# Kernel optimization log

Hardware: AMD Instinct MI355X
Metric: run time of the kernel (lower is better)

The kernel has to match this reference:

```python
import jax, jax.numpy as jnp
import numpy as np

NUM_HEADS = 16
THETA = 10000.0

def _apply_rope(x, positions):
    # x: [B, H, S, dh] with interleaved pairs; positions: [B, S] int
    dh = x.shape[-1]
    inv_freq = THETA ** (-jnp.arange(0, dh, 2, dtype=jnp.float32) / dh)  # [dh/2]
    ang = positions.astype(jnp.float32)[:, None, :, None] * inv_freq  # [B,1,S,dh/2]
    cos, sin = jnp.cos(ang), jnp.sin(ang)
    x1, x2 = x[..., 0::2], x[..., 1::2]
    out_even = x1 * cos - x2 * sin
    out_odd = x1 * sin + x2 * cos
    return jnp.stack([out_even, out_odd], axis=-1).reshape(x.shape)

def setup_inputs() -> dict:
    B, S, D = 2, 2048, 2048
    key = jax.random.key(0)
    ks = jax.random.split(key, 5)
    scale = 0.02
    inp = {
        'in_features': jax.random.normal(ks[0], (B, S, D), dtype=jnp.float32),
        'token_positions': jnp.broadcast_to(jnp.arange(S, dtype=jnp.int32), (B, S)),
        'mask': jnp.tril(jnp.ones((S, S), dtype=bool)),
        'q_proj_weight': jax.random.normal(ks[1], (D, D), dtype=jnp.float32) * scale,
        'k_proj_weight': jax.random.normal(ks[2], (D, D), dtype=jnp.float32) * scale,
        'v_proj_weight': jax.random.normal(ks[3], (D, D), dtype=jnp.float32) * scale,
        'o_proj_weight': jax.random.normal(ks[4], (D, D), dtype=jnp.float32) * scale,
    }
    return inp

def reference(in_features, token_positions, mask, q_proj_weight, k_proj_weight, v_proj_weight, o_proj_weight):
    B, S, d_in = in_features.shape
    d_k = q_proj_weight.shape[0]
    d_v = v_proj_weight.shape[0]
    H = NUM_HEADS
    dk_head, dv_head = d_k // H, d_v // H
    Q = jnp.einsum('bsd,kd->bsk', in_features, q_proj_weight).reshape(B, S, H, dk_head).transpose(0, 2, 1, 3)
    K = jnp.einsum('bsd,kd->bsk', in_features, k_proj_weight).reshape(B, S, H, dk_head).transpose(0, 2, 1, 3)
    V = jnp.einsum('bsd,vd->bsv', in_features, v_proj_weight).reshape(B, S, H, dv_head).transpose(0, 2, 1, 3)
    Q = _apply_rope(Q, token_positions)
    K = _apply_rope(K, token_positions)
    scores = jnp.einsum('bhqd,bhkd->bhqk', Q, K) / jnp.sqrt(jnp.float32(dk_head))
    scores = jnp.where(mask[None, None, :, :], scores, jnp.finfo(scores.dtype).min)
    attn = jax.nn.softmax(scores, axis=-1)
    out = jnp.einsum('bhqk,bhkd->bhqd', attn, V)  # [B,H,S,dv_head]
    out = out.transpose(0, 2, 1, 3).reshape(B, S, d_v)
    return jnp.einsum('bsv,mv->bsm', out, o_proj_weight)
```

## Files before the change

kernel.cpp:

```cpp
#include <hip/hip_runtime.h>
#include <hip/hip_bf16.h>
#include <cstdint>

typedef __bf16 bf16_t;
typedef __bf16 bf16x8 __attribute__((ext_vector_type(8)));
typedef __bf16 bf16x4 __attribute__((ext_vector_type(4)));
typedef float  f32x4  __attribute__((ext_vector_type(4)));

#define B_  2
#define S_  2048
#define D_  2048
#define H_  16
#define DH_ 128
#define LDQ 6144

__device__ __forceinline__ void gload_lds16(const bf16_t* g, bf16_t* l) {
    __builtin_amdgcn_global_load_lds(
        (const __attribute__((address_space(1))) void*)g,
        (__attribute__((address_space(3))) void*)l, 16, 0, 0);
}

#define BAR  do { asm volatile("" ::: "memory"); __builtin_amdgcn_s_barrier(); \
                  asm volatile("" ::: "memory"); } while (0)
#define WAITLGKM do { asm volatile("s_waitcnt lgkmcnt(0)" ::: "memory"); \
                      __builtin_amdgcn_sched_barrier(0); } while (0)

__global__ __launch_bounds__(256)
void cast_all_k(const float* __restrict__ X,  const float* __restrict__ Wq,
                const float* __restrict__ Wk, const float* __restrict__ Wv,
                const float* __restrict__ Wo,
                bf16_t* __restrict__ Xb, bf16_t* __restrict__ Wqkv,
                bf16_t* __restrict__ Wob) {
    long bid = blockIdx.x;
    const float* src; bf16_t* dst; long off;
    if      (bid <  8192) { src = X;  dst = Xb;             off = bid;         }
    else if (bid < 12288) { src = Wq; dst = Wqkv;           off = bid - 8192;  }
    else if (bid < 16384) { src = Wk; dst = Wqkv + 4194304; off = bid - 12288; }
    else if (bid < 20480) { src = Wv; dst = Wqkv + 8388608; off = bid - 16384; }
    else                  { src = Wo; dst = Wob;            off = bid - 20480; }
    long i = (off * 256 + threadIdx.x) * 4;
    float4 v = *(const float4*)(src + i);
    bf16x4 o = {(bf16_t)v.x, (bf16_t)v.y, (bf16_t)v.z, (bf16_t)v.w};
    *(bf16x4*)(dst + i) = o;
}

#define LDS8(s, row, chunk) \
    (*(const bf16x8*)((s) + (row) * 64 + ((((chunk) ^ ((row) & 7))) << 3)))

#define MMQ(mh, nh, bfx) \
    _Pragma("unroll") for (int mi = 0; mi < 4; ++mi) { \
      _Pragma("unroll") for (int ni = 0; ni < 2; ++ni) { \
        _Pragma("unroll") for (int ks = 0; ks < 2; ++ks) \
          acc[(mh)*4+mi][(nh)*2+ni] = __builtin_amdgcn_mfma_f32_16x16x32_bf16( \
              af[mi][ks], bfx[ni][ks], acc[(mh)*4+mi][(nh)*2+ni], 0, 0, 0); } }

__device__ __forceinline__ void ktile8(
    const bf16_t* sAc, const bf16_t* sBc,
    bf16_t* sAn, bf16_t* sBn,
    bool do_stage, long k0s,
    const bf16_t* Agp, const bf16_t* Bgp, int lda, int ldb,
    int wm, int wn, int fr, int hi, int w,
    f32x4 acc[8][4]) {
    bf16x8 af[4][2], bf0[2][2], bf1[2][2];
#pragma unroll
    for (int mi = 0; mi < 4; ++mi)
#pragma unroll
        for (int ks = 0; ks < 2; ++ks)
            af[mi][ks] = LDS8(sAc, wm * 128 + mi * 16 + fr, ks * 4 + hi);
#pragma unroll
    for (int ni = 0; ni < 2; ++ni)
#pragma unroll
        for (int ks = 0; ks < 2; ++ks)
            bf0[ni][ks] = LDS8(sBc, wn * 64 + ni * 16 + fr, ks * 4 + hi);
    if (do_stage) {
#pragma unroll
        for (int p = 0; p < 4; ++p)
            gload_lds16(Agp + (long)(p * 64) * lda + k0s, sAn + p * 4096 + w * 512);
    }
    BAR; WAITLGKM;
    __builtin_amdgcn_s_setprio(1);
    MMQ(0, 0, bf0);
    __builtin_amdgcn_s_setprio(0);
    BAR;
#pragma unroll
    for (int ni = 0; ni < 2; ++ni)
#pragma unroll
        for (int ks = 0; ks < 2; ++ks)
            bf1[ni][ks] = LDS8(sBc, wn * 64 + 32 + ni * 16 + fr, ks * 4 + hi);
    if (do_stage) {
#pragma unroll
        for (int p = 0; p < 4; ++p)
            gload_lds16(Bgp + (long)(p * 64) * ldb + k0s, sBn + p * 4096 + w * 512);
    }
    BAR; WAITLGKM;
    __builtin_amdgcn_s_setprio(1);
    MMQ(0, 1, bf1);
    __builtin_amdgcn_s_setprio(0);
    BAR;
#pragma unroll
    for (int mi = 0; mi < 4; ++mi)
#pragma unroll
        for (int ks = 0; ks < 2; ++ks)
            af[mi][ks] = LDS8(sAc, wm * 128 + 64 + mi * 16 + fr, ks * 4 + hi);
    BAR; WAITLGKM;
    __builtin_amdgcn_s_setprio(1);
    MMQ(1, 0, bf0);
    __builtin_amdgcn_s_setprio(0);
    BAR;
    __builtin_amdgcn_s_setprio(1);
    MMQ(1, 1, bf1);
    __builtin_amdgcn_s_setprio(0);
    if (do_stage) asm volatile("s_waitcnt vmcnt(0)" ::: "memory");
    BAR;
}

template<bool C_BF16>
__global__ __launch_bounds__(512, 1)
void gemm_nt8(const bf16_t* __restrict__ A, int lda,
              const bf16_t* __restrict__ B, int ldb,
              void* __restrict__ Cp, int ldc, int K, int nbx) {
    __shared__ bf16_t sA[2][256 * 64];
    __shared__ bf16_t sB[2][256 * 64];
    const int tid  = threadIdx.x;
    const int w    = tid >> 6;
    const int lane = tid & 63;
    const int fr   = lane & 15;
    const int hi   = lane >> 4;
    const int wm   = w >> 2;
    const int wn   = w & 3;

    const int nwg = gridDim.x;
    const int lin = blockIdx.x;
    const int swz = (lin & 7) * (nwg >> 3) + (lin >> 3);
    const long bm = (long)(swz / nbx) * 256;
    const long bn = (long)(swz % nbx) * 256;

    const int  srow = tid >> 3;
    const int  scol = ((tid & 7) ^ (srow & 7)) * 8;
    const bf16_t* Agp = A + (bm + srow) * (long)lda + scol;
    const bf16_t* Bgp = B + (bn + srow) * (long)ldb + scol;

    f32x4 acc[8][4] = {};
    const int nkt = K >> 6;

#pragma unroll
    for (int p = 0; p < 4; ++p)
        gload_lds16(Agp + (long)(p * 64) * lda, sA[0] + p * 4096 + w * 512);
#pragma unroll
    for (int p = 0; p < 4; ++p)
        gload_lds16(Bgp + (long)(p * 64) * ldb, sB[0] + p * 4096 + w * 512);
    asm volatile("s_waitcnt vmcnt(0)" ::: "memory");
    BAR;

    for (int kt = 0; kt < nkt; kt += 2) {
        ktile8(sA[0], sB[0], sA[1], sB[1], true, (long)(kt + 1) << 6,
               Agp, Bgp, lda, ldb, wm, wn, fr, hi, w, acc);
        ktile8(sA[1], sB[1], sA[0], sB[0], (kt + 2) < nkt, (long)(kt + 2) << 6,
               Agp, Bgp, lda, ldb, wm, wn, fr, hi, w, acc);
    }

#pragma unroll
    for (int m = 0; m < 8; ++m) {
        long r0 = bm + wm * 128 + m * 16 + hi * 4;
#pragma unroll
        for (int n = 0; n < 4; ++n) {
            long cc = bn + wn * 64 + n * 16 + fr;
#pragma unroll
            for (int v = 0; v < 4; ++v) {
                if (C_BF16)
                    ((bf16_t*)Cp)[(r0 + v) * (long)ldc + cc] = (bf16_t)acc[m][n][v];
                else
                    ((float*)Cp)[(r0 + v) * (long)ldc + cc] = acc[m][n][v];
            }
        }
    }
}

__global__ __launch_bounds__(256)
void rope_qk_k(bf16_t* __restrict__ QKV, const int* __restrict__ pos) {
    int t = blockIdx.x * 256 + threadIdx.x;
    int g = t & 15;
    int h = (t >> 4) & 15;
    int s = (t >> 8) & 2047;
    int b = t >> 19;
    long qa = ((long)(b * S_ + s)) * LDQ + h * DH_ + g * 8;
    long ka = qa + D_;
    float p = (float)pos[b * S_ + s];
    bf16x8 q = *(bf16x8*)(QKV + qa);
    bf16x8 k = *(bf16x8*)(QKV + ka);
#pragma unroll
    for (int e = 0; e < 4; ++e) {
        int i = g * 4 + e;
        float invf = exp2f(-(float)i * 0.20762050593045702f);
        float ang = p * invf;
        float sn, cs;
        __sincosf(ang, &sn, &cs);
        float q1 = (float)q[2 * e], q2 = (float)q[2 * e + 1];
        q[2 * e]     = (bf16_t)(q1 * cs - q2 * sn);
        q[2 * e + 1] = (bf16_t)(q1 * sn + q2 * cs);
        float k1 = (float)k[2 * e], k2 = (float)k[2 * e + 1];
        k[2 * e]     = (bf16_t)(k1 * cs - k2 * sn);
        k[2 * e + 1] = (bf16_t)(k1 * sn + k2 * cs);
    }
    *(bf16x8*)(QKV + qa) = q;
    *(bf16x8*)(QKV + ka) = k;
}

__global__ __launch_bounds__(256)
void transpose_v_k(const bf16_t* __restrict__ QKV, bf16_t* __restrict__ Vt) {
    __shared__ bf16_t tile[64][80];
    int t = threadIdx.x;
    int bh = blockIdx.z;
    int b = bh >> 4, h = bh & 15;
    long s0 = (long)blockIdx.x * 64;
    int d0 = blockIdx.y * 64;
    const bf16_t* src = QKV + ((long)b * S_ + s0) * LDQ + 2 * D_ + h * DH_ + d0;
#pragma unroll
    for (int p = 0; p < 2; ++p) {
        int r = (t >> 3) + p * 32;
        int c = (t & 7) * 8;
        *(bf16x8*)&tile[r][c] = *(const bf16x8*)&src[(long)r * LDQ + c];
    }
    __syncthreads();
    bf16_t* dst = Vt + ((long)bh * DH_ + d0) * S_ + s0;
#pragma unroll
    for (int p = 0; p < 2; ++p) {
        int d = (t >> 3) + p * 32;
        int c = (t & 7) * 8;
        bf16x8 v;
#pragma unroll
        for (int e = 0; e < 8; ++e) v[e] = tile[c + e][d];
        *(bf16x8*)&dst[(long)d * S_ + c] = v;
    }
}

__device__ __forceinline__ bf16x8 ldsw(const bf16_t* p, int row, int ecol) {
    return *(const bf16x8*)(p + row * 128 + (ecol ^ ((row & 7) << 3)));
}

__global__ __launch_bounds__(512, 1)
void flash_attn_k(const bf16_t* __restrict__ QKV, const bf16_t* __restrict__ Vt,
                  bf16_t* __restrict__ O) {
    __shared__ bf16_t Ksh[2][128 * 128];
    __shared__ bf16_t Vsh[2][128 * 128];
    __shared__ bf16_t Psh[128 * 128];

    const int tid  = threadIdx.x;
    const int w    = tid >> 6;
    const int lane = tid & 63;
    const int fr   = lane & 15;
    const int hi   = lane >> 4;
    const int hi8  = hi * 8;
    const int hi4  = hi * 4;
    const int w16  = w * 16;

    const int bid = blockIdx.x;
    const int qi  = 15 - (bid >> 5);
    const int bh  = bid & 31;
    const int b   = bh >> 4;
    const int h   = bh & 15;
    const long bS   = (long)b * S_;
    const int  qoff = h * DH_;
    const int  koff = D_ + h * DH_;
    const long vbase = (long)bh * DH_;

#pragma unroll
    for (int p = 0; p < 4; ++p) {
        int idx = p * 512 + tid;
        int row = idx >> 4;
        int sl  = (idx & 15) ^ (row & 7);
        gload_lds16(QKV + (bS + qi * 128 + row) * (long)LDQ + qoff + sl * 8,
                    &Psh[(p * 512 + w * 64) * 8]);
    }
#pragma unroll
    for (int p = 0; p < 4; ++p) {
        int idx = p * 512 + tid;
        int row = idx >> 4;
        int sl  = (idx & 15) ^ (row & 7);
        gload_lds16(QKV + (bS + row) * (long)LDQ + koff + sl * 8,
                    &Ksh[0][(p * 512 + w * 64) * 8]);
        gload_lds16(Vt + (vbase + row) * S_ + sl * 8,
                    &Vsh[0][(p * 512 + w * 64) * 8]);
    }
    asm volatile("s_waitcnt vmcnt(8)" ::: "memory");
    __builtin_amdgcn_s_barrier();
    asm volatile("" ::: "memory");

    bf16x8 qfrag[4];
#pragma unroll
    for (int kk = 0; kk < 4; ++kk)
        qfrag[kk] = ldsw(Psh, w16 + fr, kk * 32 + hi8);

    f32x4 o[8] = {};
    float m_run[4] = {-3.0e38f, -3.0e38f, -3.0e38f, -3.0e38f};
    float l_run[4] = {};

    const float SC = 0.08838834764831845f * 1.4426950408889634f;

    for (int kt = 0; kt <= qi; ++kt) {
        const int buf = kt & 1;
        if (kt < qi) {
#pragma unroll
            for (int p = 0; p < 4; ++p) {
                int idx = p * 512 + tid;
                int row = idx >> 4;
                int sl  = (idx & 15) ^ (row & 7);
                gload_lds16(QKV + (bS + (kt + 1) * 128 + row) * (long)LDQ + koff + sl * 8,
                            &Ksh[buf ^ 1][(p * 512 + w * 64) * 8]);
                gload_lds16(Vt + (vbase + row) * S_ + (kt + 1) * 128 + sl * 8,
                            &Vsh[buf ^ 1][(p * 512 + w * 64) * 8]);
            }
            asm volatile("s_waitcnt vmcnt(8)" ::: "memory");
        } else {
            asm volatile("s_waitcnt vmcnt(0)" ::: "memory");
        }
        __builtin_amdgcn_s_barrier();
        asm volatile("" ::: "memory");

        f32x4 sc[8];
#pragma unroll
        for (int j = 0; j < 8; ++j) {
            f32x4 z = {};
#pragma unroll
            for (int kk = 0; kk < 4; ++kk)
                z = __builtin_amdgcn_mfma_f32_16x16x32_bf16(
                        qfrag[kk], ldsw(Ksh[buf], j * 16 + fr, kk * 32 + hi8), z, 0, 0, 0);
            sc[j] = z;
        }

        const bool diag = (kt == qi);
#pragma unroll
        for (int j = 0; j < 8; ++j)
#pragma unroll
            for (int v = 0; v < 4; ++v) {
                float x = sc[j][v] * SC;
                if (diag && (j * 16 + fr > w16 + hi4 + v)) x = -3.0e38f;
                sc[j][v] = x;
            }

        float fsc[4];
#pragma unroll
        for (int v = 0; v < 4; ++v) {
            float m = fmaxf(fmaxf(fmaxf(sc[0][v], sc[1][v]), fmaxf(sc[2][v], sc[3][v])),
                            fmaxf(fmaxf(sc[4][v], sc[5][v]), fmaxf(sc[6][v], sc[7][v])));
            m = fmaxf(m, __shfl_xor(m, 1));
            m = fmaxf(m, __shfl_xor(m, 2));
            m = fmaxf(m, __shfl_xor(m, 4));
            m = fmaxf(m, __shfl_xor(m, 8));
            float mn = fmaxf(m_run[v], m);
            fsc[v] = exp2f(m_run[v] - mn);
            m_run[v] = mn;
            l_run[v] *= fsc[v];
        }
#pragma unroll
        for (int j2 = 0; j2 < 8; ++j2)
#pragma unroll
            for (int v = 0; v < 4; ++v) o[j2][v] *= fsc[v];

#pragma unroll
        for (int j = 0; j < 8; ++j)
#pragma unroll
            for (int v = 0; v < 4; ++v) {
                float p = exp2f(sc[j][v] - m_run[v]);
                l_run[v] += p;
                int row = w16 + hi4 + v;
                int col = j * 16 + fr;
                Psh[row * 128 + (col ^ ((row & 7) << 3))] = (bf16_t)p;
            }

        asm volatile("s_waitcnt lgkmcnt(0)" ::: "memory");
        __builtin_amdgcn_sched_barrier(0);

        bf16x8 pa[4];
#pragma unroll
        for (int kk = 0; kk < 4; ++kk)
            pa[kk] = ldsw(Psh, w16 + fr, kk * 32 + hi8);
#pragma unroll
        for (int j2 = 0; j2 < 8; ++j2)
#pragma unroll
            for (int kk = 0; kk < 4; ++kk)
                o[j2] = __builtin_amdgcn_mfma_f32_16x16x32_bf16(
                            pa[kk], ldsw(Vsh[buf], j2 * 16 + fr, kk * 32 + hi8), o[j2], 0, 0, 0);

        asm volatile("" ::: "memory");
        __builtin_amdgcn_s_barrier();
        asm volatile("" ::: "memory");
    }

#pragma unroll
    for (int v = 0; v < 4; ++v) {
        float l = l_run[v];
        l += __shfl_xor(l, 1);
        l += __shfl_xor(l, 2);
        l += __shfl_xor(l, 4);
        l += __shfl_xor(l, 8);
        l_run[v] = 1.0f / l;
    }
    const long orow = bS + qi * 128 + w16 + hi4;
#pragma unroll
    for (int j2 = 0; j2 < 8; ++j2)
#pragma unroll
        for (int v = 0; v < 4; ++v)
            O[(orow + v) * D_ + qoff + j2 * 16 + fr] = (bf16_t)(o[j2][v] * l_run[v]);
}

extern "C" void kernel_launch(void* const* d_in, const int* in_sizes, int n_in,
                              void* d_out, int out_size, void* d_ws, size_t ws_size,
                              hipStream_t stream) {
    const float* in_features = (const float*)d_in[0];
    const int*   positions   = (const int*)d_in[1];
    const float* Wq = (const float*)d_in[3];
    const float* Wk = (const float*)d_in[4];
    const float* Wv = (const float*)d_in[5];
    const float* Wo = (const float*)d_in[6];
    float* out = (float*)d_out;

    const size_t SZ_X   = (size_t)B_ * S_ * D_ * 2;
    const size_t SZ_W   = (size_t)D_ * D_ * 2;
    const size_t SZ_QKV = (size_t)B_ * S_ * LDQ * 2;
    if (ws_size < SZ_X * 3 + SZ_W * 4 + SZ_QKV) return;

    char* w = (char*)d_ws;
    bf16_t* Xb      = (bf16_t*)w;   w += SZ_X;
    bf16_t* Wqkv    = (bf16_t*)w;   w += SZ_W * 3;
    bf16_t* Wob     = (bf16_t*)w;   w += SZ_W;
    bf16_t* QKV     = (bf16_t*)w;   w += SZ_QKV;
    bf16_t* Vt      = (bf16_t*)w;   w += SZ_X;
    bf16_t* AttnOut = (bf16_t*)w;   w += SZ_X;

    cast_all_k<<<24576, 256, 0, stream>>>(in_features, Wq, Wk, Wv, Wo, Xb, Wqkv, Wob);

    gemm_nt8<true><<<384, 512, 0, stream>>>(Xb, D_, Wqkv, D_, QKV, LDQ, D_, 24);

    rope_qk_k<<<4096, 256, 0, stream>>>(QKV, positions);
    transpose_v_k<<<dim3(32, 2, 32), 256, 0, stream>>>(QKV, Vt);

    flash_attn_k<<<512, 512, 0, stream>>>(QKV, Vt, AttnOut);

    gemm_nt8<false><<<128, 512, 0, stream>>>(AttnOut, D_, Wob, D_, out, D_, D_, 8);
}
```

Before: 425.9 us.

## Split GEMM tile staging into finer quarter-tile prefetches and retile output projection

Replaces the two-tile ktile8 GEMM with a templated kernel that issues global-to-LDS loads in half-tile pieces spread across the four MFMA phases. A wait on all but the two most recent loads replaces the full vmcnt(0) wait, so loads can stay in flight across iterations. The output projection GEMM changes to a 256x128 tile with 4x2 warps and 256 blocks, giving more workgroups to fill the CUs. The finer-grained buffer reuse depends on the barrier and waitcnt ordering, which adds a risk of races on the LDS buffers.

```diff
diff --git a/kernel.cpp b/kernel.cpp
--- a/kernel.cpp
+++ b/kernel.cpp
@@ -47,123 +47,148 @@
 #define LDS8(s, row, chunk) \
     (*(const bf16x8*)((s) + (row) * 64 + ((((chunk) ^ ((row) & 7))) << 3)))
 
-#define MMQ(mh, nh, bfx) \
-    _Pragma("unroll") for (int mi = 0; mi < 4; ++mi) { \
-      _Pragma("unroll") for (int ni = 0; ni < 2; ++ni) { \
-        _Pragma("unroll") for (int ks = 0; ks < 2; ++ks) \
-          acc[(mh)*4+mi][(nh)*2+ni] = __builtin_amdgcn_mfma_f32_16x16x32_bf16( \
-              af[mi][ks], bfx[ni][ks], acc[(mh)*4+mi][(nh)*2+ni], 0, 0, 0); } }
-
-__device__ __forceinline__ void ktile8(
-    const bf16_t* sAc, const bf16_t* sBc,
-    bf16_t* sAn, bf16_t* sBn,
-    bool do_stage, long k0s,
-    const bf16_t* Agp, const bf16_t* Bgp, int lda, int ldb,
-    int wm, int wn, int fr, int hi, int w,
-    f32x4 acc[8][4]) {
-    bf16x8 af[4][2], bf0[2][2], bf1[2][2];
-#pragma unroll
-    for (int mi = 0; mi < 4; ++mi)
-#pragma unroll
-        for (int ks = 0; ks < 2; ++ks)
-            af[mi][ks] = LDS8(sAc, wm * 128 + mi * 16 + fr, ks * 4 + hi);
-#pragma unroll
-    for (int ni = 0; ni < 2; ++ni)
-#pragma unroll
-        for (int ks = 0; ks < 2; ++ks)
-            bf0[ni][ks] = LDS8(sBc, wn * 64 + ni * 16 + fr, ks * 4 + hi);
-    if (do_stage) {
-#pragma unroll
-        for (int p = 0; p < 4; ++p)
-            gload_lds16(Agp + (long)(p * 64) * lda + k0s, sAn + p * 4096 + w * 512);
-    }
-    BAR; WAITLGKM;
-    __builtin_amdgcn_s_setprio(1);
-    MMQ(0, 0, bf0);
-    __builtin_amdgcn_s_setprio(0);
-    BAR;
-#pragma unroll
-    for (int ni = 0; ni < 2; ++ni)
-#pragma unroll
-        for (int ks = 0; ks < 2; ++ks)
-            bf1[ni][ks] = LDS8(sBc, wn * 64 + 32 + ni * 16 + fr, ks * 4 + hi);
-    if (do_stage) {
-#pragma unroll
-        for (int p = 0; p < 4; ++p)
-            gload_lds16(Bgp + (long)(p * 64) * ldb + k0s, sBn + p * 4096 + w * 512);
-    }
-    BAR; WAITLGKM;
-    __builtin_amdgcn_s_setprio(1);
-    MMQ(0, 1, bf1);
-    __builtin_amdgcn_s_setprio(0);
-    BAR;
-#pragma unroll
-    for (int mi = 0; mi < 4; ++mi)
-#pragma unroll
-        for (int ks = 0; ks < 2; ++ks)
-            af[mi][ks] = LDS8(sAc, wm * 128 + 64 + mi * 16 + fr, ks * 4 + hi);
-    BAR; WAITLGKM;
-    __builtin_amdgcn_s_setprio(1);
-    MMQ(1, 0, bf0);
-    __builtin_amdgcn_s_setprio(0);
-    BAR;
-    __builtin_amdgcn_s_setprio(1);
-    MMQ(1, 1, bf1);
-    __builtin_amdgcn_s_setprio(0);
-    if (do_stage) asm volatile("s_waitcnt vmcnt(0)" ::: "memory");
-    BAR;
-}
-
-template<bool C_BF16>
+template<bool C_BF16, int BM, int BN, int WMG, int WNG>
 __global__ __launch_bounds__(512, 1)
-void gemm_nt8(const bf16_t* __restrict__ A, int lda,
+void gemm_nt9(const bf16_t* __restrict__ A, int lda,
               const bf16_t* __restrict__ B, int ldb,
               void* __restrict__ Cp, int ldc, int K, int nbx) {
-    __shared__ bf16_t sA[2][256 * 64];
-    __shared__ bf16_t sB[2][256 * 64];
+    constexpr int WTM = BM / WMG;
+    constexpr int MR  = WTM / 16;
+    constexpr int NR  = 4;
+    constexpr int MH  = MR / 2;
+    constexpr int NH  = 2;
+    constexpr int LA  = BM / 128;
+    constexpr int LB  = BN / 128;
+    __shared__ bf16_t sA[2][BM * 64];
+    __shared__ bf16_t sB[2][BN * 64];
+
     const int tid  = threadIdx.x;
     const int w    = tid >> 6;
     const int lane = tid & 63;
     const int fr   = lane & 15;
     const int hi   = lane >> 4;
-    const int wm   = w >> 2;
-    const int wn   = w & 3;
+    const int wm   = w / WNG;
+    const int wn   = w % WNG;
 
     const int nwg = gridDim.x;
     const int lin = blockIdx.x;
     const int swz = (lin & 7) * (nwg >> 3) + (lin >> 3);
-    const long bm = (long)(swz / nbx) * 256;
-    const long bn = (long)(swz % nbx) * 256;
-
-    const int  srow = tid >> 3;
-    const int  scol = ((tid & 7) ^ (srow & 7)) * 8;
+    const long bm = (long)(swz / nbx) * BM;
+    const long bn = (long)(swz % nbx) * BN;
+
+    const int srow = tid >> 3;
+    const int scol = ((tid & 7) ^ (srow & 7)) * 8;
     const bf16_t* Agp = A + (bm + srow) * (long)lda + scol;
     const bf16_t* Bgp = B + (bn + srow) * (long)ldb + scol;
 
-    f32x4 acc[8][4] = {};
+#define STAGE_A(bsel, h, kt) { _Pragma("unroll") \
+    for (int p = 0; p < LA; ++p) \
+        gload_lds16(Agp + (long)((h) * (BM / 2) + p * 64) * lda + ((long)(kt) << 6), \
+                    &sA[bsel][((h) * (BM / 2) + p * 64) * 64 + w * 512]); }
+#define STAGE_B(bsel, h, kt) { _Pragma("unroll") \
+    for (int p = 0; p < LB; ++p) \
+        gload_lds16(Bgp + (long)((h) * (BN / 2) + p * 64) * ldb + ((long)(kt) << 6), \
+                    &sB[bsel][((h) * (BN / 2) + p * 64) * 64 + w * 512]); }
+
+    f32x4 acc[MR][NR] = {};
     const int nkt = K >> 6;
 
-#pragma unroll
-    for (int p = 0; p < 4; ++p)
-        gload_lds16(Agp + (long)(p * 64) * lda, sA[0] + p * 4096 + w * 512);
-#pragma unroll
-    for (int p = 0; p < 4; ++p)
-        gload_lds16(Bgp + (long)(p * 64) * ldb, sB[0] + p * 4096 + w * 512);
-    asm volatile("s_waitcnt vmcnt(0)" ::: "memory");
+    STAGE_A(0, 0, 0) STAGE_A(0, 1, 0)
+    STAGE_B(0, 0, 0) STAGE_B(0, 1, 0)
+    if (nkt > 1) STAGE_A(1, 0, 1)
+    asm volatile("s_waitcnt vmcnt(2)" ::: "memory");
     BAR;
 
-    for (int kt = 0; kt < nkt; kt += 2) {
-        ktile8(sA[0], sB[0], sA[1], sB[1], true, (long)(kt + 1) << 6,
-               Agp, Bgp, lda, ldb, wm, wn, fr, hi, w, acc);
-        ktile8(sA[1], sB[1], sA[0], sB[0], (kt + 2) < nkt, (long)(kt + 2) << 6,
-               Agp, Bgp, lda, ldb, wm, wn, fr, hi, w, acc);
-    }
-
-#pragma unroll
-    for (int m = 0; m < 8; ++m) {
-        long r0 = bm + wm * 128 + m * 16 + hi * 4;
-#pragma unroll
-        for (int n = 0; n < 4; ++n) {
+    for (int t = 0; t < nkt; ++t) {
+        const int c = t & 1;
+        const bf16_t* sAc = sA[c];
+        const bf16_t* sBc = sB[c];
+        const bool st1 = t + 1 < nkt;
+        const bool st2 = t + 2 < nkt;
+        bf16x8 af[MH][2], ag[MH][2], bf0[NH][2], bf1[NH][2];
+
+#pragma unroll
+        for (int mi = 0; mi < MH; ++mi)
+#pragma unroll
+            for (int ks = 0; ks < 2; ++ks)
+                af[mi][ks] = LDS8(sAc, wm * WTM + mi * 16 + fr, ks * 4 + hi);
+#pragma unroll
+        for (int ni = 0; ni < NH; ++ni)
+#pragma unroll
+            for (int ks = 0; ks < 2; ++ks)
+                bf0[ni][ks] = LDS8(sBc, wn * 64 + ni * 16 + fr, ks * 4 + hi);
+        if (st1) STAGE_A(c ^ 1, 1, t + 1)
+        BAR; WAITLGKM;
+        __builtin_amdgcn_s_setprio(1);
+#pragma unroll
+        for (int mi = 0; mi < MH; ++mi)
+#pragma unroll
+            for (int ni = 0; ni < NH; ++ni)
+#pragma unroll
+                for (int ks = 0; ks < 2; ++ks)
+                    acc[mi][ni] = __builtin_amdgcn_mfma_f32_16x16x32_bf16(
+                        af[mi][ks], bf0[ni][ks], acc[mi][ni], 0, 0, 0);
+        __builtin_amdgcn_s_setprio(0);
+        BAR;
+
+#pragma unroll
+        for (int ni = 0; ni < NH; ++ni)
+#pragma unroll
+            for (int ks = 0; ks < 2; ++ks)
+                bf1[ni][ks] = LDS8(sBc, wn * 64 + 32 + ni * 16 + fr, ks * 4 + hi);
+        if (st1) STAGE_B(c ^ 1, 0, t + 1)
+        BAR; WAITLGKM;
+        __builtin_amdgcn_s_setprio(1);
+#pragma unroll
+        for (int mi = 0; mi < MH; ++mi)
+#pragma unroll
+            for (int ni = 0; ni < NH; ++ni)
+#pragma unroll
+                for (int ks = 0; ks < 2; ++ks)
+                    acc[mi][NH + ni] = __builtin_amdgcn_mfma_f32_16x16x32_bf16(
+                        af[mi][ks], bf1[ni][ks], acc[mi][NH + ni], 0, 0, 0);
+        __builtin_amdgcn_s_setprio(0);
+        BAR;
+
+#pragma unroll
+        for (int mi = 0; mi < MH; ++mi)
+#pragma unroll
+            for (int ks = 0; ks < 2; ++ks)
+                ag[mi][ks] = LDS8(sAc, wm * WTM + (MH + mi) * 16 + fr, ks * 4 + hi);
+        if (st1) STAGE_B(c ^ 1, 1, t + 1)
+        BAR; WAITLGKM;
+        __builtin_amdgcn_s_setprio(1);
+#pragma unroll
+        for (int mi = 0; mi < MH; ++mi)
+#pragma unroll
+            for (int ni = 0; ni < NH; ++ni)
+#pragma unroll
+                for (int ks = 0; ks < 2; ++ks)
+                    acc[MH + mi][ni] = __builtin_amdgcn_mfma_f32_16x16x32_bf16(
+                        ag[mi][ks], bf0[ni][ks], acc[MH + mi][ni], 0, 0, 0);
+        __builtin_amdgcn_s_setprio(0);
+        BAR;
+
+        if (st2) STAGE_A(c, 0, t + 2)
+        __builtin_amdgcn_s_setprio(1);
+#pragma unroll
+        for (int mi = 0; mi < MH; ++mi)
+#pragma unroll
+            for (int ni = 0; ni < NH; ++ni)
+#pragma unroll
+                for (int ks = 0; ks < 2; ++ks)
+                    acc[MH + mi][NH + ni] = __builtin_amdgcn_mfma_f32_16x16x32_bf16(
+                        ag[mi][ks], bf1[ni][ks], acc[MH + mi][NH + ni], 0, 0, 0);
+        __builtin_amdgcn_s_setprio(0);
+        asm volatile("s_waitcnt vmcnt(2)" ::: "memory");
+        BAR;
+    }
+
+#pragma unroll
+    for (int m = 0; m < MR; ++m) {
+        long r0 = bm + wm * WTM + m * 16 + hi * 4;
+#pragma unroll
+        for (int n = 0; n < NR; ++n) {
             long cc = bn + wn * 64 + n * 16 + fr;
 #pragma unroll
             for (int v = 0; v < 4; ++v) {
@@ -174,6 +199,8 @@
             }
         }
     }
+#undef STAGE_A
+#undef STAGE_B
 }
 
 __global__ __launch_bounds__(256)
@@ -430,12 +457,14 @@
 
     cast_all_k<<<24576, 256, 0, stream>>>(in_features, Wq, Wk, Wv, Wo, Xb, Wqkv, Wob);
 
-    gemm_nt8<true><<<384, 512, 0, stream>>>(Xb, D_, Wqkv, D_, QKV, LDQ, D_, 24);
+    gemm_nt9<true, 256, 256, 2, 4><<<384, 512, 0, stream>>>(Xb, D_, Wqkv, D_,
+                                                            QKV, LDQ, D_, 24);
 
     rope_qk_k<<<4096, 256, 0, stream>>>(QKV, positions);
     transpose_v_k<<<dim3(32, 2, 32), 256, 0, stream>>>(QKV, Vt);
 
     flash_attn_k<<<512, 512, 0, stream>>>(QKV, Vt, AttnOut);
 
-    gemm_nt8<false><<<128, 512, 0, stream>>>(AttnOut, D_, Wob, D_, out, D_, D_, 8);
-}
+    gemm_nt9<false, 256, 128, 4, 2><<<256, 512, 0, stream>>>(AttnOut, D_, Wob, D_,
+                                                             out, D_, D_, 16);
+}
```

Measured after the change: 407.7 us. 4.3% less time.

## Restructure GEMM into per-k-tile loop with deeper staged prefetch and half-tile LDS

Applied to the files above, without the earlier changes.

Rewrites the bf16 GEMM main loop so each k-tile is processed in four MFMA quadrants, with global-to-LDS staging for tile t+2 issued into the buffer just consumed rather than t+1. LDS is split into half-tiles per warp row/column group, and the wait on outstanding loads becomes vmcnt(8) so one tile of prefetch stays in flight. The explicit lgkmcnt waits are removed, leaving barriers only. This aims to hide global load latency better and overlap it with MFMA work, at the risk of overwriting LDS still being read if the barrier ordering is insufficient.

```diff
diff --git a/kernel.cpp b/kernel.cpp
--- a/kernel.cpp
+++ b/kernel.cpp
@@ -22,8 +22,6 @@
 
 #define BAR  do { asm volatile("" ::: "memory"); __builtin_amdgcn_s_barrier(); \
                   asm volatile("" ::: "memory"); } while (0)
-#define WAITLGKM do { asm volatile("s_waitcnt lgkmcnt(0)" ::: "memory"); \
-                      __builtin_amdgcn_sched_barrier(0); } while (0)
 
 __global__ __launch_bounds__(256)
 void cast_all_k(const float* __restrict__ X,  const float* __restrict__ Wq,
@@ -47,80 +45,14 @@
 #define LDS8(s, row, chunk) \
     (*(const bf16x8*)((s) + (row) * 64 + ((((chunk) ^ ((row) & 7))) << 3)))
 
-#define MMQ(mh, nh, bfx) \
-    _Pragma("unroll") for (int mi = 0; mi < 4; ++mi) { \
-      _Pragma("unroll") for (int ni = 0; ni < 2; ++ni) { \
-        _Pragma("unroll") for (int ks = 0; ks < 2; ++ks) \
-          acc[(mh)*4+mi][(nh)*2+ni] = __builtin_amdgcn_mfma_f32_16x16x32_bf16( \
-              af[mi][ks], bfx[ni][ks], acc[(mh)*4+mi][(nh)*2+ni], 0, 0, 0); } }
-
-__device__ __forceinline__ void ktile8(
-    const bf16_t* sAc, const bf16_t* sBc,
-    bf16_t* sAn, bf16_t* sBn,
-    bool do_stage, long k0s,
-    const bf16_t* Agp, const bf16_t* Bgp, int lda, int ldb,
-    int wm, int wn, int fr, int hi, int w,
-    f32x4 acc[8][4]) {
-    bf16x8 af[4][2], bf0[2][2], bf1[2][2];
-#pragma unroll
-    for (int mi = 0; mi < 4; ++mi)
-#pragma unroll
-        for (int ks = 0; ks < 2; ++ks)
-            af[mi][ks] = LDS8(sAc, wm * 128 + mi * 16 + fr, ks * 4 + hi);
-#pragma unroll
-    for (int ni = 0; ni < 2; ++ni)
-#pragma unroll
-        for (int ks = 0; ks < 2; ++ks)
-            bf0[ni][ks] = LDS8(sBc, wn * 64 + ni * 16 + fr, ks * 4 + hi);
-    if (do_stage) {
-#pragma unroll
-        for (int p = 0; p < 4; ++p)
-            gload_lds16(Agp + (long)(p * 64) * lda + k0s, sAn + p * 4096 + w * 512);
-    }
-    BAR; WAITLGKM;
-    __builtin_amdgcn_s_setprio(1);
-    MMQ(0, 0, bf0);
-    __builtin_amdgcn_s_setprio(0);
-    BAR;
-#pragma unroll
-    for (int ni = 0; ni < 2; ++ni)
-#pragma unroll
-        for (int ks = 0; ks < 2; ++ks)
-            bf1[ni][ks] = LDS8(sBc, wn * 64 + 32 + ni * 16 + fr, ks * 4 + hi);
-    if (do_stage) {
-#pragma unroll
-        for (int p = 0; p < 4; ++p)
-            gload_lds16(Bgp + (long)(p * 64) * ldb + k0s, sBn + p * 4096 + w * 512);
-    }
-    BAR; WAITLGKM;
-    __builtin_amdgcn_s_setprio(1);
-    MMQ(0, 1, bf1);
-    __builtin_amdgcn_s_setprio(0);
-    BAR;
-#pragma unroll
-    for (int mi = 0; mi < 4; ++mi)
-#pragma unroll
-        for (int ks = 0; ks < 2; ++ks)
-            af[mi][ks] = LDS8(sAc, wm * 128 + 64 + mi * 16 + fr, ks * 4 + hi);
-    BAR; WAITLGKM;
-    __builtin_amdgcn_s_setprio(1);
-    MMQ(1, 0, bf0);
-    __builtin_amdgcn_s_setprio(0);
-    BAR;
-    __builtin_amdgcn_s_setprio(1);
-    MMQ(1, 1, bf1);
-    __builtin_amdgcn_s_setprio(0);
-    if (do_stage) asm volatile("s_waitcnt vmcnt(0)" ::: "memory");
-    BAR;
-}
-
 template<bool C_BF16>
 __global__ __launch_bounds__(512, 1)
-void gemm_nt8(const bf16_t* __restrict__ A, int lda,
-              const bf16_t* __restrict__ B, int ldb,
-              void* __restrict__ Cp, int ldc, int K, int nbx) {
-    __shared__ bf16_t sA[2][256 * 64];
-    __shared__ bf16_t sB[2][256 * 64];
+void gemm8(const bf16_t* __restrict__ A, int lda,
+           const bf16_t* __restrict__ B, int ldb,
+           void* __restrict__ Cp, int ldc, int K, int nbx) {
+    __shared__ bf16_t sA[2][2][128 * 64];
+    __shared__ bf16_t sB[2][2][128 * 64];
+
     const int tid  = threadIdx.x;
     const int w    = tid >> 6;
     const int lane = tid & 63;
@@ -128,6 +60,8 @@
     const int hi   = lane >> 4;
     const int wm   = w >> 2;
     const int wn   = w & 3;
+    const int bh2  = wn >> 1;
+    const int brow = (wn & 1) * 64;
 
     const int nwg = gridDim.x;
     const int lin = blockIdx.x;
@@ -135,28 +69,91 @@
     const long bm = (long)(swz / nbx) * 256;
     const long bn = (long)(swz % nbx) * 256;
 
-    const int  srow = tid >> 3;
-    const int  scol = ((tid & 7) ^ (srow & 7)) * 8;
+    const int srow = tid >> 3;
+    const int scol = ((tid & 7) ^ (srow & 7)) * 8;
     const bf16_t* Agp = A + (bm + srow) * (long)lda + scol;
     const bf16_t* Bgp = B + (bn + srow) * (long)ldb + scol;
 
+#define STAGE_A2(c, kt) { _Pragma("unroll") \
+    for (int h2 = 0; h2 < 2; ++h2) { _Pragma("unroll") \
+      for (int p = 0; p < 2; ++p) \
+        gload_lds16(Agp + (long)(h2 * 128 + p * 64) * lda + ((long)(kt) << 6), \
+                    &sA[c][h2][(p * 64) * 64 + w * 512]); } }
+#define STAGE_B2(c, kt) { _Pragma("unroll") \
+    for (int h2 = 0; h2 < 2; ++h2) { _Pragma("unroll") \
+      for (int p = 0; p < 2; ++p) \
+        gload_lds16(Bgp + (long)(h2 * 128 + p * 64) * ldb + ((long)(kt) << 6), \
+                    &sB[c][h2][(p * 64) * 64 + w * 512]); } }
+
+#define MM16(am, bm_, m0, n0) { _Pragma("unroll") \
+    for (int mi = 0; mi < 4; ++mi) { _Pragma("unroll") \
+      for (int ni = 0; ni < 2; ++ni) { _Pragma("unroll") \
+        for (int ks = 0; ks < 2; ++ks) \
+          acc[(m0) + mi][(n0) + ni] = __builtin_amdgcn_mfma_f32_16x16x32_bf16( \
+              am[mi][ks], bm_[ni][ks], acc[(m0) + mi][(n0) + ni], 0, 0, 0); } } }
+
     f32x4 acc[8][4] = {};
     const int nkt = K >> 6;
 
-#pragma unroll
-    for (int p = 0; p < 4; ++p)
-        gload_lds16(Agp + (long)(p * 64) * lda, sA[0] + p * 4096 + w * 512);
-#pragma unroll
-    for (int p = 0; p < 4; ++p)
-        gload_lds16(Bgp + (long)(p * 64) * ldb, sB[0] + p * 4096 + w * 512);
-    asm volatile("s_waitcnt vmcnt(0)" ::: "memory");
+    STAGE_A2(0, 0) STAGE_B2(0, 0)
+    STAGE_A2(1, 1) STAGE_B2(1, 1)
+    asm volatile("s_waitcnt vmcnt(8)" ::: "memory");
     BAR;
 
-    for (int kt = 0; kt < nkt; kt += 2) {
-        ktile8(sA[0], sB[0], sA[1], sB[1], true, (long)(kt + 1) << 6,
-               Agp, Bgp, lda, ldb, wm, wn, fr, hi, w, acc);
-        ktile8(sA[1], sB[1], sA[0], sB[0], (kt + 2) < nkt, (long)(kt + 2) << 6,
-               Agp, Bgp, lda, ldb, wm, wn, fr, hi, w, acc);
+    for (int t = 0; t < nkt; ++t) {
+        const int c = t & 1;
+        const bool st2 = t + 2 < nkt;
+        const bf16_t* sAh = sA[c][wm];
+        const bf16_t* sBh = sB[c][bh2];
+        bf16x8 alo[4][2], ahi[4][2], blo[2][2], bhi[2][2];
+
+#pragma unroll
+        for (int mi = 0; mi < 4; ++mi)
+#pragma unroll
+            for (int ks = 0; ks < 2; ++ks)
+                alo[mi][ks] = LDS8(sAh, mi * 16 + fr, ks * 4 + hi);
+#pragma unroll
+        for (int ni = 0; ni < 2; ++ni)
+#pragma unroll
+            for (int ks = 0; ks < 2; ++ks)
+                blo[ni][ks] = LDS8(sBh, brow + ni * 16 + fr, ks * 4 + hi);
+        BAR;
+        __builtin_amdgcn_s_setprio(1);
+        MM16(alo, blo, 0, 0);
+        __builtin_amdgcn_s_setprio(0);
+        BAR;
+
+#pragma unroll
+        for (int ni = 0; ni < 2; ++ni)
+#pragma unroll
+            for (int ks = 0; ks < 2; ++ks)
+                bhi[ni][ks] = LDS8(sBh, brow + (2 + ni) * 16 + fr, ks * 4 + hi);
+        BAR;
+        __builtin_amdgcn_s_setprio(1);
+        MM16(alo, bhi, 0, 2);
+        __builtin_amdgcn_s_setprio(0);
+        BAR;
+
+#pragma unroll
+        for (int mi = 0; mi < 4; ++mi)
+#pragma unroll
+            for (int ks = 0; ks < 2; ++ks)
+                ahi[mi][ks] = LDS8(sAh, (4 + mi) * 16 + fr, ks * 4 + hi);
+        if (st2) STAGE_B2(c, t + 2)
+        BAR;
+        __builtin_amdgcn_s_setprio(1);
+        MM16(ahi, bhi, 4, 2);
+        __builtin_amdgcn_s_setprio(0);
+        BAR;
+
+        if (st2) STAGE_A2(c, t + 2)
+        BAR;
+        __builtin_amdgcn_s_setprio(1);
+        MM16(ahi, blo, 4, 0);
+        __builtin_amdgcn_s_setprio(0);
+        if (st2) { asm volatile("s_waitcnt vmcnt(8)" ::: "memory"); }
+        else     { asm volatile("s_waitcnt vmcnt(0)" ::: "memory"); }
+        BAR;
     }
 
 #pragma unroll
@@ -174,6 +171,9 @@
             }
         }
     }
+#undef STAGE_A2
+#undef STAGE_B2
+#undef MM16
 }
 
 __global__ __launch_bounds__(256)
@@ -430,12 +430,12 @@
 
     cast_all_k<<<24576, 256, 0, stream>>>(in_features, Wq, Wk, Wv, Wo, Xb, Wqkv, Wob);
 
-    gemm_nt8<true><<<384, 512, 0, stream>>>(Xb, D_, Wqkv, D_, QKV, LDQ, D_, 24);
+    gemm8<true><<<384, 512, 0, stream>>>(Xb, D_, Wqkv, D_, QKV, LDQ, D_, 24);
 
     rope_qk_k<<<4096, 256, 0, stream>>>(QKV, positions);
     transpose_v_k<<<dim3(32, 2, 32), 256, 0, stream>>>(QKV, Vt);
 
     flash_attn_k<<<512, 512, 0, stream>>>(QKV, Vt, AttnOut);
 
-    gemm_nt8<false><<<128, 512, 0, stream>>>(AttnOut, D_, Wob, D_, out, D_, D_, 8);
-}
+    gemm8<false><<<128, 512, 0, stream>>>(AttnOut, D_, Wob, D_, out, D_, D_, 8);
+}
```

Result: no change. 431.9 us (+1.4%).
